# Performance work log

Hardware: AMD Instinct MI355X
Metric: run time of the kernel (lower is better)

## Reference

```python
import jax, jax.numpy as jnp
import numpy as np

EPS = 1e-6
NUM_HEADS = 16

def _rmsnorm(h, w):
    hf = h.astype(jnp.float32)
    var = jnp.mean(hf * hf, axis=-1, keepdims=True)
    return (w * (hf * jax.lax.rsqrt(var + EPS))).astype(h.dtype)

def _rotary(t, cos, sin):
    # t: [B,N,H,hd]; cos/sin: [N, hd//2]
    tf = t.astype(jnp.float32)
    tr = tf[..., 0::2]
    ti = tf[..., 1::2]
    c = cos[None, :, None, :]
    s = sin[None, :, None, :]
    out_r = tr * c - ti * s
    out_i = tr * s + ti * c
    out = jnp.stack([out_r, out_i], axis=-1).reshape(t.shape)
    return out.astype(t.dtype)

def setup_inputs() -> dict:
    key = jax.random.key(0)
    ks = jax.random.split(key, 8)
    B, N, C = 2, 2048, 1024
    hd = C // NUM_HEADS
    x = jax.random.normal(ks[0], (B, N, C), jnp.float32)
    qkv_w = jax.random.normal(ks[1], (3 * C, C), jnp.float32) * (C ** -0.5)
    q_norm_w = jnp.ones((hd,), jnp.float32)
    k_norm_w = jnp.ones((hd,), jnp.float32)
    proj_w = jax.random.normal(ks[2], (C, C), jnp.float32) * (C ** -0.5)
    proj_b = jnp.zeros((C,), jnp.float32)
    # rotary freqs_cis = exp(i * theta): unit-magnitude cos/sin
    inv_freq = 1.0 / (10000.0 ** (jnp.arange(0, hd, 2, dtype=jnp.float32) / hd))
    ang = jnp.arange(N, dtype=jnp.float32)[:, None] * inv_freq[None, :]
    pos_cos = jnp.cos(ang)
    pos_sin = jnp.sin(ang)
    mask = jnp.tril(jnp.ones((N, N), dtype=bool))
    return {"x": x, "qkv_w": qkv_w, "q_norm_w": q_norm_w, "k_norm_w": k_norm_w,
            "proj_w": proj_w, "proj_b": proj_b, "pos_cos": pos_cos,
            "pos_sin": pos_sin, "mask": mask}

def reference(x, qkv_w, q_norm_w, k_norm_w, proj_w, proj_b, pos_cos, pos_sin, mask):
    B, N, C = x.shape
    H = NUM_HEADS
    hd = C // H
    qkv = (x @ qkv_w.T).reshape(B, N, 3, H, hd)
    q, k, v = qkv[:, :, 0], qkv[:, :, 1], qkv[:, :, 2]  # [B,N,H,hd]
    q = _rmsnorm(q, q_norm_w)
    k = _rmsnorm(k, k_norm_w)
    q = _rotary(q, pos_cos, pos_sin)
    k = _rotary(k, pos_cos, pos_sin)
    q = q.transpose(0, 2, 1, 3)  # [B,H,N,hd]
    k = k.transpose(0, 2, 1, 3)
    v = v.transpose(0, 2, 1, 3)
    scale = hd ** -0.5
    scores = jnp.einsum('bhqd,bhkd->bhqk', q, k) * scale
    scores = jnp.where(mask[None, None, :, :], scores, jnp.float32(-1e30))
    attn = jax.nn.softmax(scores, axis=-1)
    out = jnp.einsum('bhqk,bhkd->bhqd', attn, v)
    out = out.transpose(0, 2, 1, 3).reshape(B, N, C)
    return out @ proj_w.T + proj_b
```

## Files before the change

### kernel.cpp

```cpp
#include <hip/hip_runtime.h>

using u16 = unsigned short;
using short4v = __attribute__((ext_vector_type(4))) short;
using short8 = __attribute__((ext_vector_type(8))) short;
using floatx4 = __attribute__((ext_vector_type(4))) float;

__device__ __forceinline__ float bf2f(u16 h) {
  union { unsigned int u; float f; } v;
  v.u = ((unsigned int)h) << 16;
  return v.f;
}
__device__ __forceinline__ u16 f2bf(float f) {
  union { float f; unsigned int u; } v;
  v.f = f;
  unsigned int u = v.u;
  return (u16)((u + 0x7FFFu + ((u >> 16) & 1u)) >> 16);
}
__device__ __forceinline__ u16 f2bf_rtz(float f) {
  union { float f; unsigned int u; } v;
  v.f = f;
  return (u16)(v.u >> 16);
}

__device__ __forceinline__ float exp2_raw(float x) {
  return __builtin_amdgcn_exp2f(x);
}
__device__ __forceinline__ float rcp_raw(float x) {
  return __builtin_amdgcn_rcpf(x);
}

typedef const __attribute__((address_space(1))) unsigned int* gas_t;
typedef __attribute__((address_space(3))) unsigned int* las_t;
__device__ __forceinline__ void gl_lds16(const u16* g, u16* l) {
  __builtin_amdgcn_global_load_lds((gas_t)(const void*)g, (las_t)(void*)l, 16,
                                   0, 0);
}

#define MFMA32 __builtin_amdgcn_mfma_f32_16x16x32_bf16

#define QSCALE 0.180336880111f

__global__ __launch_bounds__(256) void cvt_all(
    const float* __restrict__ x, const float* __restrict__ wq,
    const float* __restrict__ wp, u16* __restrict__ xb, u16* __restrict__ wqb,
    u16* __restrict__ wpb) {
  int i = blockIdx.x * 256 + threadIdx.x;
  const float* src;
  u16* dst;
  int off;
  if (i < 1048576) {
    src = x; dst = xb; off = i;
  } else if (i < 1048576 + 786432) {
    src = wq; dst = wqb; off = i - 1048576;
  } else {
    src = wp; dst = wpb; off = i - 1835008;
  }
  float4 v = ((const float4*)src)[off];
  ushort4 o;
  o.x = f2bf(v.x);
  o.y = f2bf(v.y);
  o.z = f2bf(v.z);
  o.w = f2bf(v.w);
  ((ushort4*)dst)[off] = o;
}

template <int BIAS, int OUTBF16, int MT>
__global__ __launch_bounds__(256) void gemm_nt(
    const u16* __restrict__ A, const u16* __restrict__ B,
    const float* __restrict__ bias, void* __restrict__ Cout,
    int M, int N, int K) {
  constexpr int ROWS_A = MT * 32;
  __shared__ u16 As[ROWS_A * 64];
  __shared__ u16 Bs[128 * 64];
  const int tid = threadIdx.x;
  const int lane = tid & 63;
  const int wave = tid >> 6;
  const int col = lane & 15;
  const int quad = lane >> 4;
  const int bm = blockIdx.y * ROWS_A;
  const int bn = blockIdx.x * 128;
  const int wm = (wave >> 1) * (MT * 16);
  const int wn = (wave & 1) * 64;
  const int rsw = col & 7;

  floatx4 acc[MT][4] = {};

  for (int kb = 0; kb < K; kb += 64) {
    __syncthreads();
#pragma unroll
    for (int c = tid; c < ROWS_A * 8; c += 256) {
      const int row = c >> 3, s = (c & 7) ^ (row & 7);
      gl_lds16(A + (size_t)(bm + row) * K + kb + s * 8, As + c * 8);
    }
#pragma unroll
    for (int c = tid; c < 1024; c += 256) {
      const int row = c >> 3, s = (c & 7) ^ (row & 7);
      gl_lds16(B + (size_t)(bn + row) * K + kb + s * 8, Bs + c * 8);
    }
    __syncthreads();

#pragma unroll
    for (int kk = 0; kk < 2; kk++) {
      short8 af[MT], bfr[4];
#pragma unroll
      for (int i = 0; i < MT; i++)
        af[i] = *(const short8*)(As + (wm + i * 16 + col) * 64 +
                                 ((kk * 4 + quad) ^ rsw) * 8);
#pragma unroll
      for (int i = 0; i < 4; i++)
        bfr[i] = *(const short8*)(Bs + (wn + i * 16 + col) * 64 +
                                  ((kk * 4 + quad) ^ rsw) * 8);
#pragma unroll
      for (int mi = 0; mi < MT; mi++)
#pragma unroll
        for (int ni = 0; ni < 4; ni++)
          acc[mi][ni] = MFMA32(af[mi], bfr[ni], acc[mi][ni], 0, 0, 0);
    }
  }

#pragma unroll
  for (int mi = 0; mi < MT; mi++) {
#pragma unroll
    for (int ni = 0; ni < 4; ni++) {
#pragma unroll
      for (int r = 0; r < 4; r++) {
        int row = bm + wm + mi * 16 + quad * 4 + r;
        int c = bn + wn + ni * 16 + col;
        float v = acc[mi][ni][r];
        if (BIAS) v += bias[c];
        if (OUTBF16)
          ((u16*)Cout)[(size_t)row * N + c] = f2bf(v);
        else
          ((float*)Cout)[(size_t)row * N + c] = v;
      }
    }
  }
}

__global__ __launch_bounds__(256) void gemm_qkv(
    const u16* __restrict__ A, const u16* __restrict__ B,
    const float* __restrict__ qw, const float* __restrict__ kw,
    const float* __restrict__ pcos, const float* __restrict__ psin,
    u16* __restrict__ Qb, u16* __restrict__ Kb, u16* __restrict__ Vt) {
  constexpr int K = 1024;
  __shared__ u16 As[128 * 64];
  __shared__ u16 Bs[128 * 64];
  const int tid = threadIdx.x;
  const int lane = tid & 63;
  const int wave = tid >> 6;
  const int col = lane & 15;
  const int quad = lane >> 4;
  const int bm = blockIdx.y * 128;
  const int bn = blockIdx.x * 128;
  const int wm = (wave >> 1) * 64;
  const int wn = (wave & 1) * 64;
  const int rsw = col & 7;

  floatx4 acc[4][4] = {};

  for (int kb = 0; kb < K; kb += 64) {
    __syncthreads();
#pragma unroll
    for (int c = tid; c < 1024; c += 256) {
      const int row = c >> 3, s = (c & 7) ^ (row & 7);
      gl_lds16(A + (size_t)(bm + row) * K + kb + s * 8, As + c * 8);
    }
#pragma unroll
    for (int c = tid; c < 1024; c += 256) {
      const int row = c >> 3, s = (c & 7) ^ (row & 7);
      gl_lds16(B + (size_t)(bn + row) * K + kb + s * 8, Bs + c * 8);
    }
    __syncthreads();

#pragma unroll
    for (int kk = 0; kk < 2; kk++) {
      short8 af[4], bfr[4];
#pragma unroll
      for (int i = 0; i < 4; i++)
        af[i] = *(const short8*)(As + (wm + i * 16 + col) * 64 +
                                 ((kk * 4 + quad) ^ rsw) * 8);
#pragma unroll
      for (int i = 0; i < 4; i++)
        bfr[i] = *(const short8*)(Bs + (wn + i * 16 + col) * 64 +
                                  ((kk * 4 + quad) ^ rsw) * 8);
#pragma unroll
      for (int mi = 0; mi < 4; mi++)
#pragma unroll
        for (int ni = 0; ni < 4; ni++)
          acc[mi][ni] = MFMA32(af[mi], bfr[ni], acc[mi][ni], 0, 0, 0);
    }
  }

  const int c0 = bn + wn;
  const int type = c0 >> 10;
  const int h = (c0 >> 6) & 15;
  const int b = bm >> 11;
  const int bh = b * 16 + h;
  const int nt0 = (bm & 2047) + wm;

  __syncthreads();

  if (type == 2) {
#pragma unroll
    for (int mi = 0; mi < 4; mi++) {
#pragma unroll
      for (int ni = 0; ni < 4; ni++) {
        const int d = ni * 16 + col;
        const int n0 = nt0 + mi * 16 + quad * 4;
        short4v pk;
#pragma unroll
        for (int r = 0; r < 4; r++) pk[r] = (short)f2bf(acc[mi][ni][r]);
        *(short4v*)&Vt[((size_t)(bh * 64 + d)) * 2048 + n0] = pk;
      }
    }
  } else {
    u16* const T = (wave < 2 ? As : Bs) + (wave & 1) * 4096;
    u16* const dst = type ? Kb : Qb;
    const float* const nw = type ? kw : qw;
    float wloc[4];
#pragma unroll
    for (int ni = 0; ni < 4; ni++) wloc[ni] = nw[ni * 16 + col];

#pragma unroll
    for (int mh = 0; mh < 2; mh++) {
#pragma unroll
      for (int mm = 0; mm < 2; mm++) {
        const int mi = mh * 2 + mm;
        floatx4 ss = {};
#pragma unroll
        for (int ni = 0; ni < 4; ni++)
#pragma unroll
          for (int r = 0; r < 4; r++)
            ss[r] += acc[mi][ni][r] * acc[mi][ni][r];
#pragma unroll
        for (int off = 1; off <= 8; off <<= 1)
#pragma unroll
          for (int r = 0; r < 4; r++) ss[r] += __shfl_xor(ss[r], off);
        floatx4 rn;
#pragma unroll
        for (int r = 0; r < 4; r++)
          rn[r] = rsqrtf(ss[r] * (1.0f / 64.0f) + 1e-6f);

#pragma unroll
        for (int ni = 0; ni < 4; ni++) {
          float nv[4], pv[4];
#pragma unroll
          for (int r = 0; r < 4; r++)
            nv[r] = acc[mi][ni][r] * rn[r] * wloc[ni];
#pragma unroll
          for (int r = 0; r < 4; r++) pv[r] = __shfl_xor(nv[r], 1);
#pragma unroll
          for (int r = 0; r < 4; r++) {
            const int n = nt0 + mi * 16 + quad * 4 + r;
            const float cc = pcos[n * 32 + ni * 8 + (col >> 1)];
            const float sn = psin[n * 32 + ni * 8 + (col >> 1)];
            float out = (col & 1) ? pv[r] * sn + nv[r] * cc
                                  : nv[r] * cc - pv[r] * sn;
            if (type == 0) out *= QSCALE;
            T[(mm * 16 + quad * 4 + r) * 80 + ni * 16 + col] = f2bf(out);
          }
        }
      }
      const int tl = lane >> 3;
      const int dc = (lane & 7) * 8;
#pragma unroll
      for (int i = 0; i < 4; i++) {
        short8 v = *(const short8*)&T[(i * 8 + tl) * 80 + dc];
        const int n = nt0 + mh * 32 + i * 8 + tl;
        *(short8*)&dst[((size_t)(bh * 2048 + n)) * 64 + dc] = v;
      }
    }
  }
}

__global__ __launch_bounds__(256) void attn_flash(
    const u16* __restrict__ Q, const u16* __restrict__ Kk,
    const u16* __restrict__ Vt, u16* __restrict__ O) {
  __shared__ u16 Ks[2][2][64 * 32];
  __shared__ u16 Vs[2][2][64 * 32];
  __shared__ u16 Pb[4][16 * 64];
  const int id = blockIdx.x;
  const int bh = id & 31;
  const int tile = 31 - (id >> 5);
  const int tid = threadIdx.x;
  const int lane = tid & 63;
  const int wave = tid >> 6;
  const int col = lane & 15;
  const int quad = lane >> 4;
  const int srow = tid >> 2;
  const int sswz = ((tid & 3) ^ (srow & 3)) * 8;
  const int rq = (quad ^ (col & 3)) * 8;
  const int pswz = (col & 7) << 1;

  const u16* Qh = Q + (size_t)bh * 2048 * 64;
  const u16* Kh = Kk + (size_t)bh * 2048 * 64;
  const u16* Vh = Vt + (size_t)bh * 64 * 2048;
  const int b = bh >> 4, h = bh & 15;

  const int q0 = tile * 64 + wave * 16;

  short8 aq[2];
#pragma unroll
  for (int ks = 0; ks < 2; ks++)
    aq[ks] = *(const short8*)(Qh + (size_t)(q0 + col) * 64 + ks * 32 + quad * 8);

  short8 ones;
#pragma unroll
  for (int j = 0; j < 8; j++) ones[j] = (short)0x3F80;

  floatx4 accO[4] = {};
  floatx4 lacc = {};
  const int nsteps = tile + 1;

#pragma unroll
  for (int half = 0; half < 2; half++) {
    gl_lds16(Kh + (size_t)srow * 64 + half * 32 + sswz,
             &Ks[0][half][0] + tid * 8);
    gl_lds16(Vh + (size_t)srow * 2048 + half * 32 + sswz,
             &Vs[0][half][0] + tid * 8);
  }
  __syncthreads();

  int cur = 0;
  for (int kt = 0; kt < nsteps; kt++) {
    const int j0 = kt * 64;

    if (kt + 1 < nsteps) {
      const int j1 = j0 + 64;
#pragma unroll
      for (int half = 0; half < 2; half++) {
        gl_lds16(Kh + (size_t)(j1 + srow) * 64 + half * 32 + sswz,
                 &Ks[cur ^ 1][half][0] + tid * 8);
        gl_lds16(Vh + (size_t)srow * 2048 + j1 + half * 32 + sswz,
                 &Vs[cur ^ 1][half][0] + tid * 8);
      }
    }

    floatx4 s[4] = {};
#pragma unroll
    for (int nt = 0; nt < 4; nt++) {
#pragma unroll
      for (int ks = 0; ks < 2; ks++) {
        short8 bk = *(const short8*)&Ks[cur][ks][(nt * 16 + col) * 32 + rq];
        s[nt] = MFMA32(bk, aq[ks], s[nt], 0, 0, 0);
      }
    }

    if (j0 + 63 <= q0) {
#pragma unroll
      for (int nt = 0; nt < 4; nt++) {
        short4v pk;
#pragma unroll
        for (int r = 0; r < 4; r++)
          pk[r] = (short)f2bf_rtz(exp2_raw(s[nt][r]));
        *(short4v*)&Pb[wave][col * 64 + ((nt * 4 + quad) ^ pswz) * 4] = pk;
      }
    } else {
      const int qg = q0 + col;
#pragma unroll
      for (int nt = 0; nt < 4; nt++) {
        const int jgb = j0 + nt * 16 + quad * 4;
        short4v pk;
#pragma unroll
        for (int r = 0; r < 4; r++) {
          float pv = (jgb + r <= qg) ? exp2_raw(s[nt][r]) : 0.0f;
          pk[r] = (short)f2bf_rtz(pv);
        }
        *(short4v*)&Pb[wave][col * 64 + ((nt * 4 + quad) ^ pswz) * 4] = pk;
      }
    }

    short8 ap[2];
#pragma unroll
    for (int kf = 0; kf < 2; kf++)
      ap[kf] = *(const short8*)&Pb[wave][col * 64 +
                                         ((kf * 8 + quad * 2) ^ pswz) * 4];

#pragma unroll
    for (int kf = 0; kf < 2; kf++)
      lacc = MFMA32(ap[kf], ones, lacc, 0, 0, 0);

#pragma unroll
    for (int nt = 0; nt < 4; nt++) {
#pragma unroll
      for (int kf = 0; kf < 2; kf++) {
        short8 bv = *(const short8*)&Vs[cur][kf][(nt * 16 + col) * 32 + rq];
        accO[nt] = MFMA32(ap[kf], bv, accO[nt], 0, 0, 0);
      }
    }

    __syncthreads();
    cur ^= 1;
  }

  float lrec[4];
#pragma unroll
  for (int r = 0; r < 4; r++) lrec[r] = rcp_raw(lacc[r]);

#pragma unroll
  for (int nt = 0; nt < 4; nt++) {
#pragma unroll
    for (int r = 0; r < 4; r++) {
      int qg = q0 + quad * 4 + r;
      int d = nt * 16 + col;
      O[((size_t)(b * 2048 + qg) * 16 + h) * 64 + d] =
          f2bf(accO[nt][r] * lrec[r]);
    }
  }
}

extern "C" void kernel_launch(void* const* d_in, const int* in_sizes, int n_in,
                              void* d_out, int out_size, void* d_ws,
                              size_t ws_size, hipStream_t stream) {
  const float* x = (const float*)d_in[0];
  const float* qkv_w = (const float*)d_in[1];
  const float* q_norm_w = (const float*)d_in[2];
  const float* k_norm_w = (const float*)d_in[3];
  const float* proj_w = (const float*)d_in[4];
  const float* proj_b = (const float*)d_in[5];
  const float* pos_cos = (const float*)d_in[6];
  const float* pos_sin = (const float*)d_in[7];

  char* ws = (char*)d_ws;
  u16* xb = (u16*)ws;
  u16* wqkvb = (u16*)(ws + 8388608);
  u16* wprojb = (u16*)(ws + 14680064);
  u16* Qb = (u16*)(ws + 41943040);
  u16* Kb = (u16*)(ws + 50331648);
  u16* Vt = (u16*)(ws + 58720256);
  u16* AO = (u16*)(ws + 67108864);

  cvt_all<<<8192, 256, 0, stream>>>(x, qkv_w, proj_w, xb, wqkvb, wprojb);

  gemm_qkv<<<dim3(24, 32), 256, 0, stream>>>(xb, wqkvb, q_norm_w, k_norm_w,
                                             pos_cos, pos_sin, Qb, Kb, Vt);

  attn_flash<<<dim3(1024), 256, 0, stream>>>(Qb, Kb, Vt, AO);

  gemm_nt<1, 0, 1><<<dim3(8, 128), 256, 0, stream>>>(AO, wprojb, proj_b,
                                                     (float*)d_out, 4096, 1024,
                                                     1024);
}
```

Measured before the change: 196.8 us.

## Split attention key tiles across waves and reduce partial outputs through LDS

Each wave now owns 16 keys of every 64-key tile for all 64 queries of the block, instead of owning 16 queries. P stays in registers as the A operand of 16x16x16 MFMAs, which removes the per-step P round trip through LDS. Partial O and row sums are reduced across waves at the end through LDS, with extra barriers. Swizzles on the K/V staging are removed, which may add bank conflicts, and the register footprint grows to 16 accumulator tiles, with launch bounds set to one block.

```diff
diff --git a/kernel.cpp b/kernel.cpp
--- a/kernel.cpp
+++ b/kernel.cpp
@@ -37,6 +37,15 @@
 }
 
 #define MFMA32 __builtin_amdgcn_mfma_f32_16x16x32_bf16
+__device__ __forceinline__ floatx4 mfma16(short4v a, short4v b, floatx4 c) {
+#if __has_builtin(__builtin_amdgcn_mfma_f32_16x16x16bf16_1k)
+  return __builtin_amdgcn_mfma_f32_16x16x16bf16_1k(a, b, c, 0, 0, 0);
+#else
+  short8 a8 = {a[0], a[1], a[2], a[3], 0, 0, 0, 0};
+  short8 b8 = {b[0], b[1], b[2], b[3], 0, 0, 0, 0};
+  return MFMA32(a8, b8, c, 0, 0, 0);
+#endif
+}
 
 #define QSCALE 0.180336880111f
 
@@ -273,12 +282,12 @@
   }
 }
 
-__global__ __launch_bounds__(256) void attn_flash(
+__global__ __launch_bounds__(256, 1) void attn_flash(
     const u16* __restrict__ Q, const u16* __restrict__ Kk,
     const u16* __restrict__ Vt, u16* __restrict__ O) {
   __shared__ u16 Ks[2][2][64 * 32];
   __shared__ u16 Vs[2][2][64 * 32];
-  __shared__ u16 Pb[4][16 * 64];
+  __shared__ float lsc[4][64];
   const int id = blockIdx.x;
   const int bh = id & 31;
   const int tile = 31 - (id >> 5);
@@ -288,35 +297,36 @@
   const int col = lane & 15;
   const int quad = lane >> 4;
   const int srow = tid >> 2;
-  const int sswz = ((tid & 3) ^ (srow & 3)) * 8;
-  const int rq = (quad ^ (col & 3)) * 8;
-  const int pswz = (col & 7) << 1;
+  const int spc = (tid & 3) * 8;
 
   const u16* Qh = Q + (size_t)bh * 2048 * 64;
   const u16* Kh = Kk + (size_t)bh * 2048 * 64;
   const u16* Vh = Vt + (size_t)bh * 64 * 2048;
   const int b = bh >> 4, h = bh & 15;
 
-  const int q0 = tile * 64 + wave * 16;
-
-  short8 aq[2];
-#pragma unroll
-  for (int ks = 0; ks < 2; ks++)
-    aq[ks] = *(const short8*)(Qh + (size_t)(q0 + col) * 64 + ks * 32 + quad * 8);
-
-  short8 ones;
-#pragma unroll
-  for (int j = 0; j < 8; j++) ones[j] = (short)0x3F80;
-
-  floatx4 accO[4] = {};
-  floatx4 lacc = {};
+  const int q0 = tile * 64;
   const int nsteps = tile + 1;
 
+  short4v ones4;
+#pragma unroll
+  for (int j = 0; j < 4; j++) ones4[j] = (short)0x3F80;
+
+  short8 aq[4][2];
+#pragma unroll
+  for (int qg = 0; qg < 4; qg++)
+#pragma unroll
+    for (int ks = 0; ks < 2; ks++)
+      aq[qg][ks] = *(const short8*)(Qh + (size_t)(q0 + qg * 16 + col) * 64 +
+                                    ks * 32 + quad * 8);
+
+  floatx4 accO[4][4] = {};
+  floatx4 lacc[4] = {};
+
 #pragma unroll
   for (int half = 0; half < 2; half++) {
-    gl_lds16(Kh + (size_t)srow * 64 + half * 32 + sswz,
+    gl_lds16(Kh + (size_t)srow * 64 + half * 32 + spc,
              &Ks[0][half][0] + tid * 8);
-    gl_lds16(Vh + (size_t)srow * 2048 + half * 32 + sswz,
+    gl_lds16(Vh + (size_t)srow * 2048 + half * 32 + spc,
              &Vs[0][half][0] + tid * 8);
   }
   __syncthreads();
@@ -329,82 +339,121 @@
       const int j1 = j0 + 64;
 #pragma unroll
       for (int half = 0; half < 2; half++) {
-        gl_lds16(Kh + (size_t)(j1 + srow) * 64 + half * 32 + sswz,
+        gl_lds16(Kh + (size_t)(j1 + srow) * 64 + half * 32 + spc,
                  &Ks[cur ^ 1][half][0] + tid * 8);
-        gl_lds16(Vh + (size_t)srow * 2048 + j1 + half * 32 + sswz,
+        gl_lds16(Vh + (size_t)srow * 2048 + j1 + half * 32 + spc,
                  &Vs[cur ^ 1][half][0] + tid * 8);
       }
     }
 
+    short8 ak[2];
+#pragma unroll
+    for (int ks = 0; ks < 2; ks++)
+      ak[ks] = *(const short8*)&Ks[cur][ks][(wave * 16 + col) * 32 + quad * 8];
+    short4v bv[4];
+#pragma unroll
+    for (int dg = 0; dg < 4; dg++)
+      bv[dg] = *(const short4v*)&Vs[cur][wave >> 1]
+                   [(dg * 16 + col) * 32 + (wave & 1) * 16 + quad * 4];
+
     floatx4 s[4] = {};
 #pragma unroll
-    for (int nt = 0; nt < 4; nt++) {
-#pragma unroll
-      for (int ks = 0; ks < 2; ks++) {
-        short8 bk = *(const short8*)&Ks[cur][ks][(nt * 16 + col) * 32 + rq];
-        s[nt] = MFMA32(bk, aq[ks], s[nt], 0, 0, 0);
-      }
-    }
-
-    if (j0 + 63 <= q0) {
-#pragma unroll
-      for (int nt = 0; nt < 4; nt++) {
-        short4v pk;
+    for (int qg = 0; qg < 4; qg++)
+#pragma unroll
+      for (int ks = 0; ks < 2; ks++)
+        s[qg] = MFMA32(ak[ks], aq[qg][ks], s[qg], 0, 0, 0);
+
+    short4v pa[4];
+    if (kt < tile) {
+#pragma unroll
+      for (int qg = 0; qg < 4; qg++)
 #pragma unroll
         for (int r = 0; r < 4; r++)
-          pk[r] = (short)f2bf_rtz(exp2_raw(s[nt][r]));
-        *(short4v*)&Pb[wave][col * 64 + ((nt * 4 + quad) ^ pswz) * 4] = pk;
-      }
+          pa[qg][r] = (short)f2bf_rtz(exp2_raw(s[qg][r]));
     } else {
-      const int qg = q0 + col;
-#pragma unroll
-      for (int nt = 0; nt < 4; nt++) {
-        const int jgb = j0 + nt * 16 + quad * 4;
-        short4v pk;
+      const int keyg = j0 + wave * 16 + quad * 4;
+#pragma unroll
+      for (int qg = 0; qg < 4; qg++) {
+        const int qq = q0 + qg * 16 + col;
 #pragma unroll
         for (int r = 0; r < 4; r++) {
-          float pv = (jgb + r <= qg) ? exp2_raw(s[nt][r]) : 0.0f;
-          pk[r] = (short)f2bf_rtz(pv);
+          float pv = (keyg + r <= qq) ? exp2_raw(s[qg][r]) : 0.0f;
+          pa[qg][r] = (short)f2bf_rtz(pv);
         }
-        *(short4v*)&Pb[wave][col * 64 + ((nt * 4 + quad) ^ pswz) * 4] = pk;
-      }
-    }
-
-    short8 ap[2];
-#pragma unroll
-    for (int kf = 0; kf < 2; kf++)
-      ap[kf] = *(const short8*)&Pb[wave][col * 64 +
-                                         ((kf * 8 + quad * 2) ^ pswz) * 4];
-
-#pragma unroll
-    for (int kf = 0; kf < 2; kf++)
-      lacc = MFMA32(ap[kf], ones, lacc, 0, 0, 0);
-
-#pragma unroll
-    for (int nt = 0; nt < 4; nt++) {
-#pragma unroll
-      for (int kf = 0; kf < 2; kf++) {
-        short8 bv = *(const short8*)&Vs[cur][kf][(nt * 16 + col) * 32 + rq];
-        accO[nt] = MFMA32(ap[kf], bv, accO[nt], 0, 0, 0);
-      }
-    }
+      }
+    }
+
+#pragma unroll
+    for (int qg = 0; qg < 4; qg++) lacc[qg] = mfma16(pa[qg], ones4, lacc[qg]);
+
+#pragma unroll
+    for (int dg = 0; dg < 4; dg++)
+#pragma unroll
+      for (int qg = 0; qg < 4; qg++)
+        accO[qg][dg] = mfma16(pa[qg], bv[dg], accO[qg][dg]);
 
     __syncthreads();
     cur ^= 1;
   }
 
-  float lrec[4];
-#pragma unroll
-  for (int r = 0; r < 4; r++) lrec[r] = rcp_raw(lacc[r]);
-
-#pragma unroll
-  for (int nt = 0; nt < 4; nt++) {
-#pragma unroll
-    for (int r = 0; r < 4; r++) {
-      int qg = q0 + quad * 4 + r;
-      int d = nt * 16 + col;
-      O[((size_t)(b * 2048 + qg) * 16 + h) * 64 + d] =
-          f2bf(accO[nt][r] * lrec[r]);
+  const int sbuf = cur ^ 1;
+  float* const sc0 = (float*)&Ks[sbuf][0][0];
+  float* const sc1 = (float*)&Ks[sbuf][1][0];
+  float* const sc2 = (float*)&Vs[sbuf][0][0];
+  float* const sc3 = (float*)&Vs[sbuf][1][0];
+
+  {
+    floatx4 lv = lacc[0];
+    lv = ((col & 3) == 1) ? lacc[1] : lv;
+    lv = ((col & 3) == 2) ? lacc[2] : lv;
+    lv = ((col & 3) == 3) ? lacc[3] : lv;
+    *(floatx4*)&lsc[wave][(col & 3) * 16 + quad * 4] = lv;
+  }
+
+#pragma unroll
+  for (int r = 1; r < 4; r++) {
+#pragma unroll
+    for (int w2 = 0; w2 < 4; w2++) {
+      if (wave == w2) {
+        const int dst = (w2 + r) & 3;
+        float* d = dst == 0 ? sc0 : dst == 1 ? sc1 : dst == 2 ? sc2 : sc3;
+#pragma unroll
+        for (int qg = 0; qg < 4; qg++)
+          *(floatx4*)&d[col * 64 + (((qg * 4 + quad) ^ col) & 15) * 4] =
+              accO[qg][dst];
+      }
+    }
+    __syncthreads();
+#pragma unroll
+    for (int w2 = 0; w2 < 4; w2++) {
+      if (wave == w2) {
+        const float* m = w2 == 0 ? sc0 : w2 == 1 ? sc1 : w2 == 2 ? sc2 : sc3;
+#pragma unroll
+        for (int qg = 0; qg < 4; qg++)
+          accO[qg][w2] +=
+              *(const floatx4*)&m[col * 64 +
+                                  (((qg * 4 + quad) ^ col) & 15) * 4];
+      }
+    }
+    __syncthreads();
+  }
+
+#pragma unroll
+  for (int qg = 0; qg < 4; qg++) {
+    floatx4 lt = *(const floatx4*)&lsc[0][qg * 16 + quad * 4];
+#pragma unroll
+    for (int w2 = 1; w2 < 4; w2++)
+      lt += *(const floatx4*)&lsc[w2][qg * 16 + quad * 4];
+#pragma unroll
+    for (int w2 = 0; w2 < 4; w2++) {
+      if (wave == w2) {
+#pragma unroll
+        for (int r = 0; r < 4; r++) {
+          const int qq = q0 + qg * 16 + quad * 4 + r;
+          O[((size_t)(b * 2048 + qq) * 16 + h) * 64 + w2 * 16 + col] =
+              f2bf(accO[qg][w2][r] * rcp_raw(lt[r]));
+        }
+      }
     }
   }
 }
```

Measured after the change: 210.9 us. 7.2% more time.
